# Kernel optimization log

Measured on AMD Instinct MI355X. Metric: run time of the kernel, lower is better.

The kernel has to match this reference:

```python
import jax, jax.numpy as jnp
import numpy as np

NUM_LEVELS = 21
N_GRAM_SIZE = 4
LOW, HIGH = 0.0, 20.0


def setup_inputs() -> dict:
    key = jax.random.key(0)
    k1, k2, k3 = jax.random.split(key, 3)
    B, T, C, D = 8, 256, 16, 4096
    # continuous sensor signal in [0, 20] (matches Level embedding low/high)
    x = jax.random.uniform(k1, (B, T, C), dtype=jnp.float32, minval=LOW, maxval=HIGH)
    # bipolar {-1,+1} hypervector tables (MAP VSA model used by torchhd defaults)
    level_weight = jnp.sign(jax.random.normal(k2, (NUM_LEVELS, D), dtype=jnp.float32))
    channel_weight = jnp.sign(jax.random.normal(k3, (C, D), dtype=jnp.float32))
    return {"x": x, "level_weight": level_weight, "channel_weight": channel_weight}


def _encode(x, level_weight, channel_weight):
    # Level embedding: quantize value in [LOW, HIGH] to one of NUM_LEVELS indices
    idx = jnp.round((x - LOW) / (HIGH - LOW) * (NUM_LEVELS - 1)).astype(jnp.int32)
    idx = jnp.clip(idx, 0, NUM_LEVELS - 1)
    signal = level_weight[idx]                      # [B,T,C,D]
    # bind with channel hypervectors (elementwise multiply), multiset over channels
    samples = jnp.einsum('btcd,cd->btd', signal, channel_weight)  # [B,T,D]
    # ngrams(n=4): bind n shifted (rolled along D) windows, then multiset over windows
    n = N_GRAM_SIZE
    T = samples.shape[-2]
    n_gram = None
    for i in range(n):  # fixed small loop over n-gram positions
        window = samples[:, i:T - n + 1 + i, :]     # [B, T-n+1, D]
        rolled = jnp.roll(window, n - 1 - i, axis=-1)  # permute(shifts=n-1-i)
        n_gram = rolled if n_gram is None else n_gram * rolled
    sample_hv = n_gram.sum(axis=-2)                 # [B,D]
    # hard_quantize: sign with x>0 -> +1 else -1
    return jnp.where(sample_hv > 0, 1.0, -1.0).astype(sample_hv.dtype)


def reference(x, level_weight, channel_weight):
    return _encode(x, level_weight, channel_weight)
```

## Files before the change

### kernel.cpp

```cpp
#include <hip/hip_runtime.h>
#include <stdint.h>

#define NUM_LEVELS 21
#define BB 8
#define T 256
#define C 16
#define D 4096
#define DC 32
#define COLS 35
#define IDX_STRIDE 20
#define QROWS 66
#define QSTRIDE 36

__global__ __launch_bounds__(256, 4)
void encoder_kernel(const float* __restrict__ x,
                    const float* __restrict__ lw,
                    const float* __restrict__ cw,
                    float* __restrict__ out) {
    __shared__ uint8_t  idx_lds[T * IDX_STRIDE];
    __shared__ uint32_t lwcol[COLS], cwcol[COLS];
    __shared__ uint32_t sampQ[QROWS * QSTRIDE];
    __shared__ int      part[8 * DC];

    const int tid   = threadIdx.x;
    const int b     = blockIdx.x >> 7;
    const int chunk = blockIdx.x & 127;
    const int d0    = chunk * DC;

    const float* xb = x + b * (T * C);
    #pragma unroll
    for (int k = 0; k < 4; ++k) {
        int W = tid + k * 256;
        int t = W >> 2, m = W & 3;
        const float4 v = *(const float4*)(xb + t * C + 4 * m);
        float vv[4] = {v.x, v.y, v.z, v.w};
        uint32_t pk = 0;
        #pragma unroll
        for (int e = 0; e < 4; ++e) {
            float fi = (vv[e] / 20.0f) * 20.0f;
            int id = (int)rintf(fi);
            id = min(max(id, 0), NUM_LEVELS - 1);
            pk |= (uint32_t)id << (8 * e);
        }
        *(uint32_t*)(idx_lds + t * IDX_STRIDE + 4 * m) = pk;
    }

    if (tid < COLS) {
        int d = (d0 - 3 + tid) & (D - 1);
        uint32_t wl = 0;
        #pragma unroll
        for (int l = 0; l < NUM_LEVELS; ++l)
            wl |= (__float_as_uint(lw[l * D + d]) >> 31) << l;
        lwcol[tid] = wl;
        uint32_t wc = 0;
        #pragma unroll
        for (int c = 0; c < C; ++c)
            wc |= (__float_as_uint(cw[c * D + d]) >> 31) << c;
        cwcol[tid] = wc;
    }
    __syncthreads();

    {
        const int q = tid >> 2;
        const int g = tid & 3;
        uint32_t accum[9];
        #pragma unroll
        for (int k = 0; k < 9; ++k) accum[k] = 0;
        #pragma unroll
        for (int tp = 0; tp < 4; ++tp) {
            const int t = 4 * q + tp;
            const uint32_t* row = (const uint32_t*)(idx_lds + t * IDX_STRIDE);
            uint32_t w0 = row[0], w1 = row[1], w2 = row[2], w3 = row[3];
            int l[16];
            #pragma unroll
            for (int e = 0; e < 4; ++e) {
                l[e]      = (w0 >> (8 * e)) & 31;
                l[4 + e]  = (w1 >> (8 * e)) & 31;
                l[8 + e]  = (w2 >> (8 * e)) & 31;
                l[12 + e] = (w3 >> (8 * e)) & 31;
            }
            #pragma unroll
            for (int k = 0; k < 9; ++k) {
                int col = 9 * g + k; col = col > 34 ? 34 : col;
                uint32_t lc = lwcol[col], cc = cwcol[col];
                uint32_t m = 0;
                #pragma unroll
                for (int c = 0; c < 16; ++c)
                    m |= ((lc >> l[c]) & 1u) << c;
                int s = 16 - 2 * __popc(m ^ cc);
                accum[k] |= (uint32_t)(uint8_t)(int8_t)s << (8 * tp);
            }
        }
        #pragma unroll
        for (int k = 0; k < 9; ++k) {
            int col = 9 * g + k; col = col > 34 ? 34 : col;
            sampQ[q * QSTRIDE + col] = accum[k];
        }
    }
    __syncthreads();

    const int j   = tid & 31;
    const int seg = tid >> 5;
    int acc = 0;
    {
        const int t0 = seg * 32;
        const int t1 = (t0 + 32 < 253) ? t0 + 32 : 253;
        const int q0 = t0 >> 2;
        uint32_t A[4], Bv[4];
        #pragma unroll
        for (int i = 0; i < 4; ++i) {
            A[i]  = sampQ[q0 * QSTRIDE + j + i];
            Bv[i] = sampQ[(q0 + 1) * QSTRIDE + j + i];
        }
        for (int t = t0; t < t1; t += 4) {
            uint32_t pk0 = A[0];
            uint32_t pk1 = (A[1] >> 8)  | (Bv[1] << 24);
            uint32_t pk2 = (A[2] >> 16) | (Bv[2] << 16);
            uint32_t pk3 = (A[3] >> 24) | (Bv[3] << 8);
            #pragma unroll
            for (int k = 0; k < 4; ++k) {
                if (t + k < t1) {
                    int s0 = (int)(int8_t)(pk0 >> (8 * k));
                    int s1 = (int)(int8_t)(pk1 >> (8 * k));
                    int s2 = (int)(int8_t)(pk2 >> (8 * k));
                    int s3 = (int)(int8_t)(pk3 >> (8 * k));
                    acc += (s0 * s1) * (s2 * s3);
                }
            }
            const int qn = (t >> 2) + 2;
            #pragma unroll
            for (int i = 0; i < 4; ++i) {
                A[i]  = Bv[i];
                Bv[i] = sampQ[qn * QSTRIDE + j + i];
            }
        }
    }
    if (seg) part[(seg - 1) * DC + j] = acc;
    __syncthreads();

    if (seg == 0) {
        int hv = acc;
        #pragma unroll
        for (int s = 0; s < 7; ++s) hv += part[s * DC + j];
        out[b * D + d0 + j] = hv > 0 ? 1.0f : -1.0f;
    }
}

extern "C" void kernel_launch(void* const* d_in, const int* in_sizes, int n_in,
                              void* d_out, int out_size, void* d_ws, size_t ws_size,
                              hipStream_t stream) {
    const float* x  = (const float*)d_in[0];
    const float* lw = (const float*)d_in[1];
    const float* cw = (const float*)d_in[2];
    float* out = (float*)d_out;
    dim3 grid(BB * (D / DC));
    dim3 block(256);
    encoder_kernel<<<grid, block, 0, stream>>>(x, lw, cw, out);
}
```

Measured before the change: 75.07 us.

## Split bit-packing prep into separate kernel and halve per-block D chunk

Moves the quantization of x into level indices and the bit-packing of level/channel weight columns into a separate prep kernel that writes to workspace, so they are no longer redone by every block. The encoder kernel then reads the packed indices and columns straight from global memory instead of staging them in LDS. It also halves the D chunk per block to 16, doubling the grid to 2048 blocks, with 16 time segments per column. The cost is a second kernel launch, global reads of the index rows per thread, and more redundant halo columns plus a longer partial-sum reduction per output.

```diff
diff --git a/kernel.cpp b/kernel.cpp
--- a/kernel.cpp
+++ b/kernel.cpp
@@ -6,33 +6,24 @@
 #define T 256
 #define C 16
 #define D 4096
-#define DC 32
-#define COLS 35
-#define IDX_STRIDE 20
+#define DC 16
+#define COLS 19
+#define QSTRIDE 20
 #define QROWS 66
-#define QSTRIDE 36
 
-__global__ __launch_bounds__(256, 4)
-void encoder_kernel(const float* __restrict__ x,
-                    const float* __restrict__ lw,
-                    const float* __restrict__ cw,
-                    float* __restrict__ out) {
-    __shared__ uint8_t  idx_lds[T * IDX_STRIDE];
-    __shared__ uint32_t lwcol[COLS], cwcol[COLS];
-    __shared__ uint32_t sampQ[QROWS * QSTRIDE];
-    __shared__ int      part[8 * DC];
+#define WS_IDX 0
+#define WS_LW  8192
+#define WS_CW  12288
 
-    const int tid   = threadIdx.x;
-    const int b     = blockIdx.x >> 7;
-    const int chunk = blockIdx.x & 127;
-    const int d0    = chunk * DC;
-
-    const float* xb = x + b * (T * C);
-    #pragma unroll
-    for (int k = 0; k < 4; ++k) {
-        int W = tid + k * 256;
-        int t = W >> 2, m = W & 3;
-        const float4 v = *(const float4*)(xb + t * C + 4 * m);
+__global__ __launch_bounds__(256)
+void prep_kernel(const float* __restrict__ x,
+                 const float* __restrict__ lw,
+                 const float* __restrict__ cw,
+                 uint32_t* __restrict__ ws) {
+    const int blk = blockIdx.x, tid = threadIdx.x;
+    if (blk < 32) {
+        const int W = blk * 256 + tid;
+        const float4 v = *(const float4*)(x + 4 * W);
         float vv[4] = {v.x, v.y, v.z, v.w};
         uint32_t pk = 0;
         #pragma unroll
@@ -42,69 +33,80 @@
             id = min(max(id, 0), NUM_LEVELS - 1);
             pk |= (uint32_t)id << (8 * e);
         }
-        *(uint32_t*)(idx_lds + t * IDX_STRIDE + 4 * m) = pk;
-    }
-
-    if (tid < COLS) {
-        int d = (d0 - 3 + tid) & (D - 1);
+        ws[WS_IDX + W] = pk;
+    } else {
+        const int d = (blk - 32) * 256 + tid;
         uint32_t wl = 0;
         #pragma unroll
         for (int l = 0; l < NUM_LEVELS; ++l)
             wl |= (__float_as_uint(lw[l * D + d]) >> 31) << l;
-        lwcol[tid] = wl;
+        ws[WS_LW + d] = wl;
         uint32_t wc = 0;
         #pragma unroll
         for (int c = 0; c < C; ++c)
             wc |= (__float_as_uint(cw[c * D + d]) >> 31) << c;
-        cwcol[tid] = wc;
+        ws[WS_CW + d] = wc;
     }
-    __syncthreads();
+}
+
+__global__ __launch_bounds__(256)
+void encoder_kernel(const uint32_t* __restrict__ ws,
+                    float* __restrict__ out) {
+    __shared__ uint32_t sampQ[QROWS * QSTRIDE];
+    __shared__ int      part[15 * DC];
+
+    const int tid = threadIdx.x;
+    const int b   = blockIdx.x >> 8;
+    const int d0  = (blockIdx.x & 255) * DC;
 
     {
         const int q = tid >> 2;
         const int g = tid & 3;
-        uint32_t accum[9];
+        uint32_t lc[5], cc[5];
         #pragma unroll
-        for (int k = 0; k < 9; ++k) accum[k] = 0;
+        for (int k = 0; k < 5; ++k) {
+            int col = 5 * g + k; col = col > 18 ? 18 : col;
+            int d = (d0 - 3 + col) & (D - 1);
+            lc[k] = ws[WS_LW + d];
+            cc[k] = ws[WS_CW + d];
+        }
+        uint32_t accum[5] = {0, 0, 0, 0, 0};
         #pragma unroll
         for (int tp = 0; tp < 4; ++tp) {
             const int t = 4 * q + tp;
-            const uint32_t* row = (const uint32_t*)(idx_lds + t * IDX_STRIDE);
-            uint32_t w0 = row[0], w1 = row[1], w2 = row[2], w3 = row[3];
+            const uint4 row = *(const uint4*)(ws + WS_IDX + b * 1024 + t * 4);
             int l[16];
             #pragma unroll
             for (int e = 0; e < 4; ++e) {
-                l[e]      = (w0 >> (8 * e)) & 31;
-                l[4 + e]  = (w1 >> (8 * e)) & 31;
-                l[8 + e]  = (w2 >> (8 * e)) & 31;
-                l[12 + e] = (w3 >> (8 * e)) & 31;
+                l[e]      = (row.x >> (8 * e)) & 31;
+                l[4 + e]  = (row.y >> (8 * e)) & 31;
+                l[8 + e]  = (row.z >> (8 * e)) & 31;
+                l[12 + e] = (row.w >> (8 * e)) & 31;
             }
             #pragma unroll
-            for (int k = 0; k < 9; ++k) {
-                int col = 9 * g + k; col = col > 34 ? 34 : col;
-                uint32_t lc = lwcol[col], cc = cwcol[col];
+            for (int k = 0; k < 5; ++k) {
                 uint32_t m = 0;
                 #pragma unroll
                 for (int c = 0; c < 16; ++c)
-                    m |= ((lc >> l[c]) & 1u) << c;
-                int s = 16 - 2 * __popc(m ^ cc);
+                    m |= ((lc[k] >> l[c]) & 1u) << c;
+                int s = 16 - 2 * __popc(m ^ cc[k]);
                 accum[k] |= (uint32_t)(uint8_t)(int8_t)s << (8 * tp);
             }
         }
         #pragma unroll
-        for (int k = 0; k < 9; ++k) {
-            int col = 9 * g + k; col = col > 34 ? 34 : col;
+        for (int k = 0; k < 5; ++k) {
+            int col = 5 * g + k; col = col > 18 ? 18 : col;
             sampQ[q * QSTRIDE + col] = accum[k];
         }
     }
     __syncthreads();
 
-    const int j   = tid & 31;
-    const int seg = tid >> 5;
+    const int j   = tid & 15;
+    const int seg = tid >> 4;
     int acc = 0;
     {
-        const int t0 = seg * 32;
-        const int t1 = (t0 + 32 < 253) ? t0 + 32 : 253;
+        const int t0 = seg * 16;
+        const int t1 = (t0 + 16 < 253) ? t0 + 16 : 253;
         const int q0 = t0 >> 2;
         uint32_t A[4], Bv[4];
         #pragma unroll
@@ -141,7 +143,7 @@
     if (seg == 0) {
         int hv = acc;
         #pragma unroll
-        for (int s = 0; s < 7; ++s) hv += part[s * DC + j];
+        for (int s = 0; s < 15; ++s) hv += part[s * DC + j];
         out[b * D + d0 + j] = hv > 0 ? 1.0f : -1.0f;
     }
 }
@@ -153,7 +155,8 @@
     const float* lw = (const float*)d_in[1];
     const float* cw = (const float*)d_in[2];
     float* out = (float*)d_out;
-    dim3 grid(BB * (D / DC));
-    dim3 block(256);
-    encoder_kernel<<<grid, block, 0, stream>>>(x, lw, cw, out);
+    uint32_t* ws = (uint32_t*)d_ws;
+
+    prep_kernel<<<48, 256, 0, stream>>>(x, lw, cw, ws);
+    encoder_kernel<<<BB * (D / DC), 256, 0, stream>>>(ws, out);
 }
```

Result: slower. 76.92 us (+2.5%).
